# Optimization experiments

Measured on AMD Instinct MI355X. Metric: run time of the kernel, lower is better.

Reference implementation:

```python
import jax, jax.numpy as jnp
import numpy as np

B, T = 128, 512
V, P, K = 10002, 500, 20
DC, DP, DT = 300, 100, 50
D = DC + DP + DT
H = 256


def setup_inputs() -> dict:
    key = jax.random.key(0)
    ks = jax.random.split(key, 21)
    s = lambda i, shape: jax.random.normal(ks[i], shape, jnp.float32) * 0.05
    return dict(
        x=jax.random.randint(ks[0], (B, T), 0, V),
        y=jax.random.randint(ks[1], (B, T), 0, K),
        pre_tags=jax.random.randint(ks[2], (B, T), 0, K),
        pinyin_tags=jax.random.randint(ks[3], (B, T), 0, P),
        mask=jnp.ones((B, T), bool),
        char_emb=s(4, (V, DC)),
        tag_emb=s(5, (K, DT)),
        pinyin_emb=s(6, (P, DP)),
        w_ih_f=s(7, (4 * H, D)), w_hh_f=s(8, (4 * H, H)), b_ih_f=s(9, (4 * H,)), b_hh_f=s(10, (4 * H,)),
        w_ih_b=s(11, (4 * H, D)), w_hh_b=s(12, (4 * H, H)), b_ih_b=s(13, (4 * H,)), b_hh_b=s(14, (4 * H,)),
        w_out=s(15, (K, 2 * H)), b_out=s(16, (K,)),
        start_trans=s(17, (K,)), end_trans=s(18, (K,)), trans=s(19, (K, K)),
    )


def _lstm_dir(xs, w_ih, w_hh, b_ih, b_hh, reverse):
    # xs: [T,B,D]; precompute input projection for all steps (one big GEMM)
    pre = jnp.einsum('tbd,gd->tbg', xs, w_ih) + b_ih + b_hh  # [T,B,4H]
    bsz = xs.shape[1]

    def step(carry, gx):
        h, c = carry
        g = gx + h @ w_hh.T
        i, f, gg, o = jnp.split(g, 4, axis=-1)  # torch gate order i,f,g,o
        c = jax.nn.sigmoid(f) * c + jax.nn.sigmoid(i) * jnp.tanh(gg)
        h = jax.nn.sigmoid(o) * jnp.tanh(c)
        return (h, c), h

    init = (jnp.zeros((bsz, H), xs.dtype), jnp.zeros((bsz, H), xs.dtype))
    _, hs = jax.lax.scan(step, init, pre, reverse=reverse)
    return hs  # [T,B,H]


def _emissions(x, pre_tags, pinyin_tags, char_emb, tag_emb, pinyin_emb,
               w_ih_f, w_hh_f, b_ih_f, b_hh_f, w_ih_b, w_hh_b, b_ih_b, b_hh_b,
               w_out, b_out):
    emb = jnp.concatenate([char_emb[x], pinyin_emb[pinyin_tags], tag_emb[pre_tags]], axis=2)  # [B,T,D]
    xs = emb.transpose(1, 0, 2)  # [T,B,D]
    hf = _lstm_dir(xs, w_ih_f, w_hh_f, b_ih_f, b_hh_f, reverse=False)
    hb = _lstm_dir(xs, w_ih_b, w_hh_b, b_ih_b, b_hh_b, reverse=True)
    h = jnp.concatenate([hf, hb], axis=-1)  # [T,B,2H]
    return jnp.einsum('tbh,kh->tbk', h, w_out) + b_out  # emissions [T,B,K]


def _crf_nll(em, tags, mask, start, trans, end):
    # em [T,B,K] (time-major), torchcrf forward with reduction='sum'
    tg = tags.T  # [T,B]
    mk = mask.T.astype(em.dtype)  # [T,B]
    # gold-path score
    first = start[tg[0]] + jnp.take_along_axis(em[0], tg[0][:, None], 1)[:, 0]

    def num_step(score, inputs):
        e_t, t_prev, t_cur, m = inputs
        s = trans[t_prev, t_cur] + jnp.take_along_axis(e_t, t_cur[:, None], 1)[:, 0]
        return score + s * m, None

    score, _ = jax.lax.scan(num_step, first, (em[1:], tg[:-1], tg[1:], mk[1:]))
    last_idx = (mask.sum(1) - 1).astype(jnp.int32)
    last_tag = jnp.take_along_axis(tags, last_idx[:, None].astype(tags.dtype), 1)[:, 0]
    score = score + end[last_tag]
    # partition function via forward algorithm
    alpha0 = start[None, :] + em[0]  # [B,K]

    def den_step(alpha, inputs):
        e_t, m = inputs
        nxt = jax.nn.logsumexp(alpha[:, :, None] + trans[None, :, :] + e_t[:, None, :], axis=1)
        return jnp.where(m[:, None] > 0, nxt, alpha), None

    alpha, _ = jax.lax.scan(den_step, alpha0, (em[1:], mk[1:]))
    logZ = jax.nn.logsumexp(alpha + end[None, :], axis=1)
    llh = jnp.sum(score - logZ)
    return -llh  # module returns -crf(...)


def reference(x, y, pre_tags, pinyin_tags, mask, char_emb, tag_emb, pinyin_emb,
              w_ih_f, w_hh_f, b_ih_f, b_hh_f, w_ih_b, w_hh_b, b_ih_b, b_hh_b,
              w_out, b_out, start_trans, end_trans, trans):
    em = _emissions(x, pre_tags, pinyin_tags, char_emb, tag_emb, pinyin_emb,
                    w_ih_f, w_hh_f, b_ih_f, b_hh_f, w_ih_b, w_hh_b, b_ih_b, b_hh_b,
                    w_out, b_out)
    return _crf_nll(em, y, mask, start_trans, trans, end_trans)
```

## Files before the change

kernel.cpp:

```cpp
#include <hip/hip_runtime.h>
#include <hip/hip_bf16.h>

typedef __attribute__((ext_vector_type(8))) short short8;
typedef __attribute__((ext_vector_type(4))) float float4v;

#if __has_builtin(__builtin_amdgcn_sdot4)
#define DOT4(a, b, c) __builtin_amdgcn_sdot4((int)(a), (int)(b), (c), false)
#else
__device__ __forceinline__ int dot4_(int a, int b, int c) {
  c += (int)(signed char)(a) * (int)(signed char)(b);
  c += (int)(signed char)(a >> 8) * (int)(signed char)(b >> 8);
  c += (int)(signed char)(a >> 16) * (int)(signed char)(b >> 16);
  c += (a >> 24) * (b >> 24);
  return c;
}
#define DOT4(a, b, c) dot4_((int)(a), (int)(b), (c))
#endif

__device__ __forceinline__ float sigmoidf_(float x) {
  return __fdividef(1.f, 1.f + __expf(-x));
}
__device__ __forceinline__ float tanhf_(float x) {
  float e = __expf(2.f * x);
  return 1.f - __fdividef(2.f, e + 1.f);
}
__device__ __forceinline__ float bflo(unsigned int v) {
  return __uint_as_float(v << 16);
}
__device__ __forceinline__ float bfhi(unsigned int v) {
  return __uint_as_float(v & 0xffff0000u);
}
__device__ __forceinline__ void barrier_lgkm() {
  asm volatile("s_waitcnt lgkmcnt(0)\n\ts_barrier" ::: "memory");
}

template <int CTRL>
__device__ __forceinline__ int qadd_i(int v) {
  return v + __builtin_amdgcn_update_dpp(0, v, CTRL, 0xF, 0xF, true);
}
#define XOR1 0xB1
#define XOR2 0x4E

__device__ __forceinline__ unsigned int pack4_(float4 v, float inv) {
  int b0 = (int)rintf(v.x * inv), b1 = (int)rintf(v.y * inv);
  int b2 = (int)rintf(v.z * inv), b3 = (int)rintf(v.w * inv);
  return (unsigned int)((b0 & 0xff) | ((b1 & 0xff) << 8) | ((b2 & 0xff) << 16) |
                        ((b3 & 0xff) << 24));
}

__global__ __launch_bounds__(256) void wquant_kernel(
    const float* __restrict__ whh_f, const float* __restrict__ whh_b,
    unsigned int* __restrict__ wq, float* __restrict__ wsc) {
  const int wave_g = blockIdx.x * 4 + (threadIdx.x >> 6);
  const int lane = threadIdx.x & 63;
  const int dir = wave_g >> 10, row = wave_g & 1023;
  const float* __restrict__ src = (dir ? whh_b : whh_f) + (size_t)row * 256;
  float4 v = ((const float4*)src)[lane];
  float mx = fmaxf(fmaxf(fabsf(v.x), fabsf(v.y)), fmaxf(fabsf(v.z), fabsf(v.w)));
#pragma unroll
  for (int k = 32; k >= 1; k >>= 1) mx = fmaxf(mx, __shfl_xor(mx, k, 64));
  float inv = (mx > 0.f) ? __fdividef(127.f, mx) : 0.f;
  wq[(size_t)wave_g * 64 + lane] = pack4_(v, inv);
  if (lane == 0) wsc[wave_g] = (mx > 0.f) ? (mx / (127.f * 127.f)) : 0.f;
}

__global__ __launch_bounds__(256) void proj_gemm(
    const float* __restrict__ A, int rowsA, int Kdim, int col_off,
    const float* __restrict__ wf, const float* __restrict__ wb,
    const float* __restrict__ bf1, const float* __restrict__ bf2,
    const float* __restrict__ bb1, const float* __restrict__ bb2,
    __hip_bfloat16* __restrict__ out, int add_bias) {
  __shared__ __align__(16) __hip_bfloat16 As[128][40];
  __shared__ __align__(16) __hip_bfloat16 Bs[256][40];
  const int tid = threadIdx.x;
  const int m0 = blockIdx.x * 128, n0 = blockIdx.y * 256;
  const int lane = tid & 63, wave = tid >> 6;
  const int quad = lane >> 4, lm = lane & 15;
  float4v acc[2][16] = {};
  const int ksteps = (Kdim + 31) >> 5;
  const int r2 = tid >> 1, cbase = (tid & 1) << 4;
  const int rb = tid >> 4, cb = (tid & 15) * 2;
  for (int ks = 0; ks < ksteps; ++ks) {
    const int k0 = ks << 5;
#pragma unroll
    for (int e2 = 0; e2 < 8; ++e2) {
      int kk = k0 + cbase + 2 * e2;
      float b0 = 0.f, b1 = 0.f;
      if (m0 + r2 < rowsA && kk < Kdim) {
        float2 v = *(const float2*)(A + (size_t)(m0 + r2) * Kdim + kk);
        b0 = v.x;
        b1 = v.y;
      }
      As[r2][cbase + 2 * e2] = __float2bfloat16(b0);
      As[r2][cbase + 2 * e2 + 1] = __float2bfloat16(b1);
    }
#pragma unroll
    for (int j = 0; j < 16; ++j) {
      int n = n0 + rb + 16 * j;
      const float* __restrict__ wrow =
          (n < 1024) ? (wf + n * 450 + col_off) : (wb + (n - 1024) * 450 + col_off);
      int kk = k0 + cb;
      float b0 = 0.f, b1 = 0.f;
      if (kk < Kdim) {
        float2 v = *(const float2*)(wrow + kk);
        b0 = v.x;
        b1 = v.y;
      }
      Bs[rb + 16 * j][cb] = __float2bfloat16(b0);
      Bs[rb + 16 * j][cb + 1] = __float2bfloat16(b1);
    }
    __syncthreads();
    short8 af0 = *(const short8*)(&As[wave * 32 + lm][quad * 8]);
    short8 af1 = *(const short8*)(&As[wave * 32 + 16 + lm][quad * 8]);
#pragma unroll
    for (int t = 0; t < 16; ++t) {
      short8 bf = *(const short8*)(&Bs[t * 16 + lm][quad * 8]);
      acc[0][t] = __builtin_amdgcn_mfma_f32_16x16x32_bf16(af0, bf, acc[0][t], 0, 0, 0);
      acc[1][t] = __builtin_amdgcn_mfma_f32_16x16x32_bf16(af1, bf, acc[1][t], 0, 0, 0);
    }
    __syncthreads();
  }
#pragma unroll
  for (int mg = 0; mg < 2; ++mg) {
#pragma unroll
    for (int t = 0; t < 16; ++t) {
#pragma unroll
      for (int rr = 0; rr < 4; ++rr) {
        int m = m0 + wave * 32 + mg * 16 + quad * 4 + rr;
        int col = n0 + t * 16 + lm;
        if (m < rowsA) {
          float v = acc[mg][t][rr];
          if (add_bias)
            v += (col < 1024) ? (bf1[col] + bf2[col]) : (bb1[col - 1024] + bb2[col - 1024]);
          int dir = col >> 10, rq = col & 1023;
          int gate = rq >> 8, u = rq & 255;
          out[m * 2048 + dir * 1024 + u * 4 + gate] = __float2bfloat16(v);
        }
      }
    }
  }
}

__global__ __launch_bounds__(512, 2) void lstm_kernel(
    const unsigned int* __restrict__ wq, const float* __restrict__ wsc,
    const int* __restrict__ x, const int* __restrict__ ptags, const int* __restrict__ gtags,
    const char* __restrict__ char_proj, const char* __restrict__ pin_proj,
    const char* __restrict__ tag_proj, __hip_bfloat16* __restrict__ h_out) {
  extern __shared__ __align__(16) char smem[];
  __hip_bfloat16* hist = (__hip_bfloat16*)smem;
  signed char* hb = (signed char*)(smem + 16384);

  const int tid = threadIdx.x;
  const int q = tid >> 2, e = tid & 3;
  const int chain = blockIdx.x;
  const int dir = chain >> 7;
  const int b = chain & 127;
  const int boff = b * 512;

  if (tid < 32) ((int4*)hb)[tid] = make_int4(0, 0, 0, 0);

  int rslot = tid;
  asm volatile("" : "+v"(rslot));

  const unsigned int* __restrict__ wqd = wq + (size_t)dir * 65536;
  const float* __restrict__ wscd = wsc + dir * 1024;
  const int sub_e = e & 1;
  const int u_mine = 2 * q + sub_e;

  unsigned int Wreg[8][16];
  {
    uint4* lbuf = (uint4*)smem;
#pragma unroll
    for (int rr = 0; rr < 8; ++rr) {
      const int g = rr & 3, sub = rr >> 2;
      const int grow = g * 256 + 2 * q + sub;
      const uint4* __restrict__ srcp = (const uint4*)(wqd + grow * 64 + e * 16);
#pragma unroll
      for (int c = 0; c < 4; ++c) {
        lbuf[tid] = srcp[c];
        uint4 a = lbuf[rslot];
        Wreg[rr][4 * c + 0] = a.x;
        Wreg[rr][4 * c + 1] = a.y;
        Wreg[rr][4 * c + 2] = a.z;
        Wreg[rr][4 * c + 3] = a.w;
      }
    }
  }
  float sc4[4];
  {
    float* fl = (float*)(smem + 8192);
#pragma unroll
    for (int g = 0; g < 4; ++g) {
      fl[tid] = wscd[g * 256 + u_mine];
      sc4[g] = fl[rslot];
    }
  }
  __syncthreads();

  const int pre_off = dir * 2048 + u_mine * 8;
  float cst = 0.f;

  int t_cur = dir ? 511 : 0;
  int t_nxt = dir ? 510 : 1;
  int xc = x[boff + t_cur], pc_i = ptags[boff + t_cur], gc_i = gtags[boff + t_cur];
  uint2 vc = *(const uint2*)(char_proj + (size_t)xc * 4096 + pre_off);
  uint2 vp = *(const uint2*)(pin_proj + (size_t)pc_i * 4096 + pre_off);
  uint2 vg = *(const uint2*)(tag_proj + (size_t)gc_i * 4096 + pre_off);
  int xn = x[boff + t_nxt], pn = ptags[boff + t_nxt], gn = gtags[boff + t_nxt];

  for (int s = 0; s < 512; ++s) {
    const uint2 cv = vc, pv = vp, gv = vg;
    const int t_fut = dir ? (t_nxt > 0 ? t_nxt - 1 : 0) : (t_nxt < 511 ? t_nxt + 1 : 511);
    vc = *(const uint2*)(char_proj + (size_t)xn * 4096 + pre_off);
    vp = *(const uint2*)(pin_proj + (size_t)pn * 4096 + pre_off);
    vg = *(const uint2*)(tag_proj + (size_t)gn * 4096 + pre_off);
    xn = x[boff + t_fut];
    pn = ptags[boff + t_fut];
    gn = gtags[boff + t_fut];

    const signed char* hbase = hb + (s & 1) * 256 + e * 64;
    int acc[8] = {0, 0, 0, 0, 0, 0, 0, 0};
#pragma unroll
    for (int c = 0; c < 4; ++c) {
      uint4 H = *(const uint4*)(hbase + c * 16);
#pragma unroll
      for (int rr = 0; rr < 8; ++rr) {
        acc[rr] = DOT4(Wreg[rr][4 * c + 0], H.x, acc[rr]);
        acc[rr] = DOT4(Wreg[rr][4 * c + 1], H.y, acc[rr]);
        acc[rr] = DOT4(Wreg[rr][4 * c + 2], H.z, acc[rr]);
        acc[rr] = DOT4(Wreg[rr][4 * c + 3], H.w, acc[rr]);
      }
    }
#pragma unroll
    for (int rr = 0; rr < 8; ++rr) {
      int v = qadd_i<XOR1>(acc[rr]);
      acc[rr] = qadd_i<XOR2>(v);
    }
    int ai = sub_e ? acc[4] : acc[0];
    int af = sub_e ? acc[5] : acc[1];
    int ag = sub_e ? acc[6] : acc[2];
    int ao = sub_e ? acc[7] : acc[3];
    float gi = bflo(cv.x) + bflo(pv.x) + bflo(gv.x) + (float)ai * sc4[0];
    float gf = bfhi(cv.x) + bfhi(pv.x) + bfhi(gv.x) + (float)af * sc4[1];
    float gg = bflo(cv.y) + bflo(pv.y) + bflo(gv.y) + (float)ag * sc4[2];
    float go = bfhi(cv.y) + bfhi(pv.y) + bfhi(gv.y) + (float)ao * sc4[3];
    cst = sigmoidf_(gf) * cst + sigmoidf_(gi) * tanhf_(gg);
    float hval = sigmoidf_(go) * tanhf_(cst);
    if (e < 2) {
      hb[((s + 1) & 1) * 256 + u_mine] = (signed char)(int)rintf(hval * 127.f);
      hist[(s & 31) * 256 + u_mine] = __float2bfloat16(hval);
    }
    barrier_lgkm();
    if ((s & 15) == 15) {
      const int slotBase = (s & 31) & ~15;
      const int sBase = s - 15;
      const int row = tid >> 5;
      const int col16 = tid & 31;
      uint4 v = *(const uint4*)((const char*)hist + (slotBase + row) * 512 + col16 * 16);
      int step_r = sBase + row;
      int t_r = dir ? (511 - step_r) : step_r;
      *(uint4*)((char*)h_out + ((size_t)(chain * 512 + t_r) * 256) * 2 + col16 * 16) = v;
    }
    t_cur = t_nxt;
    t_nxt = t_fut;
  }
}

__global__ __launch_bounds__(256) void emis_kernel(
    const __hip_bfloat16* __restrict__ h_glob, const float* __restrict__ w_out,
    const float* __restrict__ b_out, float* __restrict__ em) {
  __shared__ __align__(16) __hip_bfloat16 As[64][40];
  __shared__ __align__(16) __hip_bfloat16 Bs[32][40];
  const int tid = threadIdx.x;
  const int n0 = blockIdx.x * 64;
  const int lane = tid & 63, wave = tid >> 6, quad = lane >> 4, lm = lane & 15;
  float4v acc[2] = {};
  const int r = tid >> 2, c0 = (tid & 3) << 3;
  const int rb = tid >> 3, cb = (tid & 7) << 2;
  for (int ks = 0; ks < 16; ++ks) {
    const int j0 = ks * 32;
    const int dirk = j0 >> 8, jin = j0 & 255;
    const int n = n0 + r, bb = n >> 9, tt = n & 511;
    const uint4* src =
        (const uint4*)(h_glob + ((size_t)(dirk * 128 + bb) * 512 + tt) * 256 + jin + c0);
    *(uint4*)(&As[r][c0]) = *src;
#pragma unroll
    for (int e = 0; e < 4; ++e) {
      float v = (rb < 20) ? w_out[rb * 512 + j0 + cb + e] : 0.f;
      Bs[rb][cb + e] = __float2bfloat16(v);
    }
    __syncthreads();
    short8 af = *(const short8*)(&As[wave * 16 + lm][quad * 8]);
#pragma unroll
    for (int t2 = 0; t2 < 2; ++t2) {
      short8 bf = *(const short8*)(&Bs[t2 * 16 + lm][quad * 8]);
      acc[t2] = __builtin_amdgcn_mfma_f32_16x16x32_bf16(af, bf, acc[t2], 0, 0, 0);
    }
    __syncthreads();
  }
#pragma unroll
  for (int t2 = 0; t2 < 2; ++t2) {
#pragma unroll
    for (int rr = 0; rr < 4; ++rr) {
      int col = t2 * 16 + lm;
      if (col < 20) {
        int n = n0 + wave * 16 + quad * 4 + rr;
        em[(size_t)n * 20 + col] = acc[t2][rr] + b_out[col];
      }
    }
  }
}

__global__ __launch_bounds__(64) void crf_kernel(
    const float* __restrict__ em, const int* __restrict__ y,
    const float* __restrict__ start_trans, const float* __restrict__ end_trans,
    const float* __restrict__ trans, float* __restrict__ partials) {
  const int b = blockIdx.x;
  const int lane = threadIdx.x;
  const int jj = lane < 20 ? lane : 19;
  const bool act = lane < 20;
  const float* __restrict__ emb = em + (size_t)b * 512 * 20;
  const int* __restrict__ yb = y + b * 512;

  float s_part = 0.f;
#pragma unroll
  for (int i = 0; i < 8; ++i) {
    int t = lane + 64 * i;
    int yc = yb[t];
    float v = emb[t * 20 + yc];
    v += (t == 0) ? start_trans[yc] : trans[yb[t - 1] * 20 + yc];
    s_part += v;
  }
#pragma unroll
  for (int k = 32; k >= 1; k >>= 1) s_part += __shfl_xor(s_part, k, 64);
  float score = s_part + end_trans[yb[511]];

  float ET[20];
#pragma unroll
  for (int i = 0; i < 20; ++i) ET[i] = __expf(trans[i * 20 + jj]);
  float alpha = act ? (start_trans[jj] + emb[jj]) : -1e30f;
  float P = alpha;
#pragma unroll
  for (int k = 32; k >= 1; k >>= 1) P = fmaxf(P, __shfl_xor(P, k, 64));

  float eC = emb[1 * 20 + jj];
  float eN = emb[2 * 20 + jj];
  for (int t = 1; t < 512; ++t) {
    if ((t & 15) == 0) {
      P = alpha;
#pragma unroll
      for (int k = 32; k >= 1; k >>= 1) P = fmaxf(P, __shfl_xor(P, k, 64));
    }
    float ex = __expf(alpha - P);
    float s0 = 0.f, s1 = 0.f;
#pragma unroll
    for (int i = 0; i < 20; i += 2) {
      float e0 = __int_as_float(__builtin_amdgcn_readlane(__float_as_int(ex), i));
      float e1 = __int_as_float(__builtin_amdgcn_readlane(__float_as_int(ex), i + 1));
      s0 = fmaf(e0, ET[i], s0);
      s1 = fmaf(e1, ET[i + 1], s1);
    }
    int tf = t + 2 < 512 ? t + 2 : 511;
    float eF = emb[tf * 20 + jj];
    if (act) alpha = P + __logf(s0 + s1) + eC;
    eC = eN;
    eN = eF;
  }
  float v = act ? (alpha + end_trans[jj]) : -1e30f;
  float Pz = v;
#pragma unroll
  for (int k = 32; k >= 1; k >>= 1) Pz = fmaxf(Pz, __shfl_xor(Pz, k, 64));
  float e2 = __expf(v - Pz);
#pragma unroll
  for (int k = 32; k >= 1; k >>= 1) e2 += __shfl_xor(e2, k, 64);
  float logZ = Pz + __logf(e2);
  if (lane == 0) partials[b] = logZ - score;
}

__global__ __launch_bounds__(128) void reduce_kernel(const float* __restrict__ partials,
                                                     float* __restrict__ out) {
  const int tid = threadIdx.x;
  float v = partials[tid];
#pragma unroll
  for (int k = 32; k >= 1; k >>= 1) v += __shfl_xor(v, k, 64);
  __shared__ float tmp[2];
  if ((tid & 63) == 0) tmp[tid >> 6] = v;
  __syncthreads();
  if (tid == 0) out[0] = tmp[0] + tmp[1];
}

extern "C" void kernel_launch(void* const* d_in, const int* in_sizes, int n_in,
                              void* d_out, int out_size, void* d_ws, size_t ws_size,
                              hipStream_t stream) {
  const int* x = (const int*)d_in[0];
  const int* y = (const int*)d_in[1];
  const int* pre_tags = (const int*)d_in[2];
  const int* pinyin_tags = (const int*)d_in[3];
  const float* char_emb = (const float*)d_in[5];
  const float* tag_emb = (const float*)d_in[6];
  const float* pinyin_emb = (const float*)d_in[7];
  const float* w_ih_f = (const float*)d_in[8];
  const float* w_hh_f = (const float*)d_in[9];
  const float* b_ih_f = (const float*)d_in[10];
  const float* b_hh_f = (const float*)d_in[11];
  const float* w_ih_b = (const float*)d_in[12];
  const float* w_hh_b = (const float*)d_in[13];
  const float* b_ih_b = (const float*)d_in[14];
  const float* b_hh_b = (const float*)d_in[15];
  const float* w_out = (const float*)d_in[16];
  const float* b_out = (const float*)d_in[17];
  const float* start_trans = (const float*)d_in[18];
  const float* end_trans = (const float*)d_in[19];
  const float* trans = (const float*)d_in[20];

  char* ws = (char*)d_ws;
  __hip_bfloat16* char_proj = (__hip_bfloat16*)(ws);
  __hip_bfloat16* pin_proj = (__hip_bfloat16*)(ws + 40968192);
  __hip_bfloat16* tag_proj = (__hip_bfloat16*)(ws + 43016192);
  __hip_bfloat16* h_glob = (__hip_bfloat16*)(ws + 43098112);
  float* em = (float*)(ws + 110206976);
  float* partials = (float*)(ws + 115449856);
  unsigned int* wq = (unsigned int*)(ws + 110206976);
  float* wsc = (float*)(ws + 110206976 + 524288);

  wquant_kernel<<<512, 256, 0, stream>>>(w_hh_f, w_hh_b, wq, wsc);

  proj_gemm<<<dim3(79, 8), 256, 0, stream>>>(char_emb, 10002, 300, 0, w_ih_f, w_ih_b,
                                             nullptr, nullptr, nullptr, nullptr, char_proj, 0);
  proj_gemm<<<dim3(4, 8), 256, 0, stream>>>(pinyin_emb, 500, 100, 300, w_ih_f, w_ih_b,
                                            nullptr, nullptr, nullptr, nullptr, pin_proj, 0);
  proj_gemm<<<dim3(1, 8), 256, 0, stream>>>(tag_emb, 20, 50, 400, w_ih_f, w_ih_b,
                                            b_ih_f, b_hh_f, b_ih_b, b_hh_b, tag_proj, 1);

  const int lstm_lds = 16896;
  hipFuncSetAttribute((const void*)lstm_kernel, hipFuncAttributeMaxDynamicSharedMemorySize,
                      lstm_lds);
  lstm_kernel<<<256, 512, lstm_lds, stream>>>(wq, wsc, x, pinyin_tags, pre_tags,
                                              (const char*)char_proj, (const char*)pin_proj,
                                              (const char*)tag_proj, h_glob);

  emis_kernel<<<1024, 256, 0, stream>>>(h_glob, w_out, b_out, em);
  crf_kernel<<<128, 64, 0, stream>>>(em, y, start_trans, end_trans, trans, partials);
  reduce_kernel<<<1, 128, 0, stream>>>(partials, (float*)d_out);
}
```

Baseline: 1.088 ms.

## Batch 16 LSTM chains per block using int8 MFMA for recurrent matvec

Replaces the per-chain LSTM recurrence, which used one block per sequence with sdot4 dot products and DPP reductions, with blocks that each handle 16 batch elements of one direction. The recurrent step becomes an int8 16x16x64 MFMA GEMM with weights held in MFMA fragment registers. The grid shrinks from 256 blocks to 16, so the 512 sequential steps run on far fewer CUs. In exchange each step does dense matrix work with better weight reuse, at the cost of more work per block per step and less parallelism across the device.

```diff
diff --git a/kernel.cpp b/kernel.cpp
--- a/kernel.cpp
+++ b/kernel.cpp
@@ -3,19 +3,7 @@
 
 typedef __attribute__((ext_vector_type(8))) short short8;
 typedef __attribute__((ext_vector_type(4))) float float4v;
-
-#if __has_builtin(__builtin_amdgcn_sdot4)
-#define DOT4(a, b, c) __builtin_amdgcn_sdot4((int)(a), (int)(b), (c), false)
-#else
-__device__ __forceinline__ int dot4_(int a, int b, int c) {
-  c += (int)(signed char)(a) * (int)(signed char)(b);
-  c += (int)(signed char)(a >> 8) * (int)(signed char)(b >> 8);
-  c += (int)(signed char)(a >> 16) * (int)(signed char)(b >> 16);
-  c += (a >> 24) * (b >> 24);
-  return c;
-}
-#define DOT4(a, b, c) dot4_((int)(a), (int)(b), (c))
-#endif
+typedef __attribute__((ext_vector_type(4))) int int4v;
 
 __device__ __forceinline__ float sigmoidf_(float x) {
   return __fdividef(1.f, 1.f + __expf(-x));
@@ -33,19 +21,17 @@
 __device__ __forceinline__ void barrier_lgkm() {
   asm volatile("s_waitcnt lgkmcnt(0)\n\ts_barrier" ::: "memory");
 }
-
-template <int CTRL>
-__device__ __forceinline__ int qadd_i(int v) {
-  return v + __builtin_amdgcn_update_dpp(0, v, CTRL, 0xF, 0xF, true);
-}
-#define XOR1 0xB1
-#define XOR2 0x4E
 
 __device__ __forceinline__ unsigned int pack4_(float4 v, float inv) {
   int b0 = (int)rintf(v.x * inv), b1 = (int)rintf(v.y * inv);
   int b2 = (int)rintf(v.z * inv), b3 = (int)rintf(v.w * inv);
   return (unsigned int)((b0 & 0xff) | ((b1 & 0xff) << 8) | ((b2 & 0xff) << 16) |
                         ((b3 & 0xff) << 24));
+}
+
+__device__ __forceinline__ unsigned short bf16bits_(float v) {
+  __hip_bfloat16 b = __float2bfloat16(v);
+  return *(unsigned short*)&b;
 }
 
 __global__ __launch_bounds__(256) void wquant_kernel(
@@ -147,122 +133,121 @@
     const char* __restrict__ char_proj, const char* __restrict__ pin_proj,
     const char* __restrict__ tag_proj, __hip_bfloat16* __restrict__ h_out) {
   extern __shared__ __align__(16) char smem[];
-  __hip_bfloat16* hist = (__hip_bfloat16*)smem;
-  signed char* hb = (signed char*)(smem + 16384);
+  char* hqb = smem;
+  char* histb = smem + 8704;
+  float* wscL = (float*)(smem + 42496);
 
   const int tid = threadIdx.x;
-  const int q = tid >> 2, e = tid & 3;
-  const int chain = blockIdx.x;
-  const int dir = chain >> 7;
-  const int b = chain & 127;
-  const int boff = b * 512;
-
-  if (tid < 32) ((int4*)hb)[tid] = make_int4(0, 0, 0, 0);
-
-  int rslot = tid;
-  asm volatile("" : "+v"(rslot));
+  const int w = tid >> 6, lane = tid & 63;
+  const int lm = lane & 15, quad = lane >> 4;
+  const int blk = blockIdx.x;
+  const int dir = blk >> 3, bg = blk & 7;
+  const int bb = bg * 16 + lm;
+  const int b512 = bb * 512;
+
+  for (int i = tid; i < 1024; i += 512) wscL[i] = wsc[dir * 1024 + i];
+  for (int i = tid; i < 2176; i += 512) ((unsigned int*)hqb)[i] = 0u;
 
   const unsigned int* __restrict__ wqd = wq + (size_t)dir * 65536;
-  const float* __restrict__ wscd = wsc + dir * 1024;
-  const int sub_e = e & 1;
-  const int u_mine = 2 * q + sub_e;
-
-  unsigned int Wreg[8][16];
-  {
-    uint4* lbuf = (uint4*)smem;
-#pragma unroll
-    for (int rr = 0; rr < 8; ++rr) {
-      const int g = rr & 3, sub = rr >> 2;
-      const int grow = g * 256 + 2 * q + sub;
-      const uint4* __restrict__ srcp = (const uint4*)(wqd + grow * 64 + e * 16);
-#pragma unroll
-      for (int c = 0; c < 4; ++c) {
-        lbuf[tid] = srcp[c];
-        uint4 a = lbuf[rslot];
-        Wreg[rr][4 * c + 0] = a.x;
-        Wreg[rr][4 * c + 1] = a.y;
-        Wreg[rr][4 * c + 2] = a.z;
-        Wreg[rr][4 * c + 3] = a.w;
+  int4v Wf[4][2][4];
+#pragma unroll
+  for (int g = 0; g < 4; ++g)
+#pragma unroll
+    for (int h = 0; h < 2; ++h) {
+      const int row = g * 256 + w * 32 + h * 16 + lm;
+#pragma unroll
+      for (int kt = 0; kt < 4; ++kt)
+        Wf[g][h][kt] = *(const int4v*)(wqd + row * 64 + kt * 16 + quad * 4);
+    }
+  __syncthreads();
+
+  float c8[2][4] = {};
+  const size_t preoff0 = (size_t)dir * 2048 + (size_t)(w * 32 + quad * 4) * 8;
+
+  int t = dir ? 511 : 0;
+  int xi = x[b512 + t], pi = ptags[b512 + t], gi_ = gtags[b512 + t];
+
+  for (int s = 0; s < 512; ++s) {
+    const int cur = s & 1, nxt = cur ^ 1;
+    const char* cb0 = char_proj + (size_t)xi * 4096 + preoff0;
+    const char* pb0 = pin_proj + (size_t)pi * 4096 + preoff0;
+    const char* tb0 = tag_proj + (size_t)gi_ * 4096 + preoff0;
+    uint4 pc0[2], pp0[2], pt0[2];
+    pc0[0] = *(const uint4*)(cb0);      pc0[1] = *(const uint4*)(cb0 + 16);
+    pp0[0] = *(const uint4*)(pb0);      pp0[1] = *(const uint4*)(pb0 + 16);
+    pt0[0] = *(const uint4*)(tb0);      pt0[1] = *(const uint4*)(tb0 + 16);
+    int sn = (s + 1 < 512) ? s + 1 : 511;
+    int tn = dir ? 511 - sn : sn;
+    int xin = x[b512 + tn], pin_ = ptags[b512 + tn], gin = gtags[b512 + tn];
+
+    int4v acc[4][2] = {};
+    const char* hqcur = hqb + cur * 4352 + lm * 272;
+#pragma unroll
+    for (int kt = 0; kt < 4; ++kt) {
+      int4v Bv = *(const int4v*)(hqcur + kt * 64 + quad * 16);
+#pragma unroll
+      for (int g = 0; g < 4; ++g)
+#pragma unroll
+        for (int h = 0; h < 2; ++h)
+          acc[g][h] = __builtin_amdgcn_mfma_i32_16x16x64_i8(Wf[g][h][kt], Bv, acc[g][h], 0, 0, 0);
+    }
+    uint4 pc1[2], pp1[2], pt1[2];
+    pc1[0] = *(const uint4*)(cb0 + 128); pc1[1] = *(const uint4*)(cb0 + 144);
+    pp1[0] = *(const uint4*)(pb0 + 128); pp1[1] = *(const uint4*)(pb0 + 144);
+    pt1[0] = *(const uint4*)(tb0 + 128); pt1[1] = *(const uint4*)(tb0 + 144);
+
+    char* hqn = hqb + nxt * 4352 + lm * 272 + w * 32 + quad * 4;
+    char* histp = histb + (s & 3) * 8448 + lm * 528 + (size_t)(w * 32 + quad * 4) * 2;
+
+#pragma unroll
+    for (int h = 0; h < 2; ++h) {
+      const float4 s0 = *(const float4*)&wscL[0 * 256 + w * 32 + h * 16 + quad * 4];
+      const float4 s1 = *(const float4*)&wscL[1 * 256 + w * 32 + h * 16 + quad * 4];
+      const float4 s2 = *(const float4*)&wscL[2 * 256 + w * 32 + h * 16 + quad * 4];
+      const float4 s3 = *(const float4*)&wscL[3 * 256 + w * 32 + h * 16 + quad * 4];
+      unsigned int hqpack = 0, hist0 = 0, hist1 = 0;
+#pragma unroll
+      for (int rr = 0; rr < 4; ++rr) {
+        uint4 cc = h ? pc1[rr >> 1] : pc0[rr >> 1];
+        uint4 pp = h ? pp1[rr >> 1] : pp0[rr >> 1];
+        uint4 tt = h ? pt1[rr >> 1] : pt0[rr >> 1];
+        unsigned lo_c = (rr & 1) ? cc.z : cc.x, hi_c = (rr & 1) ? cc.w : cc.y;
+        unsigned lo_p = (rr & 1) ? pp.z : pp.x, hi_p = (rr & 1) ? pp.w : pp.y;
+        unsigned lo_t = (rr & 1) ? tt.z : tt.x, hi_t = (rr & 1) ? tt.w : tt.y;
+        float sci = (rr == 0) ? s0.x : (rr == 1) ? s0.y : (rr == 2) ? s0.z : s0.w;
+        float scf = (rr == 0) ? s1.x : (rr == 1) ? s1.y : (rr == 2) ? s1.z : s1.w;
+        float scg = (rr == 0) ? s2.x : (rr == 1) ? s2.y : (rr == 2) ? s2.z : s2.w;
+        float sco = (rr == 0) ? s3.x : (rr == 1) ? s3.y : (rr == 2) ? s3.z : s3.w;
+        float vi = bflo(lo_c) + bflo(lo_p) + bflo(lo_t) + (float)acc[0][h][rr] * sci;
+        float vf = bfhi(lo_c) + bfhi(lo_p) + bfhi(lo_t) + (float)acc[1][h][rr] * scf;
+        float vg = bflo(hi_c) + bflo(hi_p) + bflo(hi_t) + (float)acc[2][h][rr] * scg;
+        float vo = bfhi(hi_c) + bfhi(hi_p) + bfhi(hi_t) + (float)acc[3][h][rr] * sco;
+        float c = sigmoidf_(vf) * c8[h][rr] + sigmoidf_(vi) * tanhf_(vg);
+        c8[h][rr] = c;
+        float hv = sigmoidf_(vo) * tanhf_(c);
+        hqpack |= ((unsigned)((int)rintf(hv * 127.f) & 0xff)) << (8 * rr);
+        unsigned hb = (unsigned)bf16bits_(hv);
+        if (rr < 2) hist0 |= hb << (16 * rr);
+        else hist1 |= hb << (16 * (rr - 2));
       }
-    }
-  }
-  float sc4[4];
-  {
-    float* fl = (float*)(smem + 8192);
-#pragma unroll
-    for (int g = 0; g < 4; ++g) {
-      fl[tid] = wscd[g * 256 + u_mine];
-      sc4[g] = fl[rslot];
-    }
-  }
-  __syncthreads();
-
-  const int pre_off = dir * 2048 + u_mine * 8;
-  float cst = 0.f;
-
-  int t_cur = dir ? 511 : 0;
-  int t_nxt = dir ? 510 : 1;
-  int xc = x[boff + t_cur], pc_i = ptags[boff + t_cur], gc_i = gtags[boff + t_cur];
-  uint2 vc = *(const uint2*)(char_proj + (size_t)xc * 4096 + pre_off);
-  uint2 vp = *(const uint2*)(pin_proj + (size_t)pc_i * 4096 + pre_off);
-  uint2 vg = *(const uint2*)(tag_proj + (size_t)gc_i * 4096 + pre_off);
-  int xn = x[boff + t_nxt], pn = ptags[boff + t_nxt], gn = gtags[boff + t_nxt];
-
-  for (int s = 0; s < 512; ++s) {
-    const uint2 cv = vc, pv = vp, gv = vg;
-    const int t_fut = dir ? (t_nxt > 0 ? t_nxt - 1 : 0) : (t_nxt < 511 ? t_nxt + 1 : 511);
-    vc = *(const uint2*)(char_proj + (size_t)xn * 4096 + pre_off);
-    vp = *(const uint2*)(pin_proj + (size_t)pn * 4096 + pre_off);
-    vg = *(const uint2*)(tag_proj + (size_t)gn * 4096 + pre_off);
-    xn = x[boff + t_fut];
-    pn = ptags[boff + t_fut];
-    gn = gtags[boff + t_fut];
-
-    const signed char* hbase = hb + (s & 1) * 256 + e * 64;
-    int acc[8] = {0, 0, 0, 0, 0, 0, 0, 0};
-#pragma unroll
-    for (int c = 0; c < 4; ++c) {
-      uint4 H = *(const uint4*)(hbase + c * 16);
-#pragma unroll
-      for (int rr = 0; rr < 8; ++rr) {
-        acc[rr] = DOT4(Wreg[rr][4 * c + 0], H.x, acc[rr]);
-        acc[rr] = DOT4(Wreg[rr][4 * c + 1], H.y, acc[rr]);
-        acc[rr] = DOT4(Wreg[rr][4 * c + 2], H.z, acc[rr]);
-        acc[rr] = DOT4(Wreg[rr][4 * c + 3], H.w, acc[rr]);
-      }
-    }
-#pragma unroll
-    for (int rr = 0; rr < 8; ++rr) {
-      int v = qadd_i<XOR1>(acc[rr]);
-      acc[rr] = qadd_i<XOR2>(v);
-    }
-    int ai = sub_e ? acc[4] : acc[0];
-    int af = sub_e ? acc[5] : acc[1];
-    int ag = sub_e ? acc[6] : acc[2];
-    int ao = sub_e ? acc[7] : acc[3];
-    float gi = bflo(cv.x) + bflo(pv.x) + bflo(gv.x) + (float)ai * sc4[0];
-    float gf = bfhi(cv.x) + bfhi(pv.x) + bfhi(gv.x) + (float)af * sc4[1];
-    float gg = bflo(cv.y) + bflo(pv.y) + bflo(gv.y) + (float)ag * sc4[2];
-    float go = bfhi(cv.y) + bfhi(pv.y) + bfhi(gv.y) + (float)ao * sc4[3];
-    cst = sigmoidf_(gf) * cst + sigmoidf_(gi) * tanhf_(gg);
-    float hval = sigmoidf_(go) * tanhf_(cst);
-    if (e < 2) {
-      hb[((s + 1) & 1) * 256 + u_mine] = (signed char)(int)rintf(hval * 127.f);
-      hist[(s & 31) * 256 + u_mine] = __float2bfloat16(hval);
+      *(unsigned int*)(hqn + h * 16) = hqpack;
+      *(uint2*)(histp + h * 32) = make_uint2(hist0, hist1);
     }
     barrier_lgkm();
-    if ((s & 15) == 15) {
-      const int slotBase = (s & 31) & ~15;
-      const int sBase = s - 15;
-      const int row = tid >> 5;
-      const int col16 = tid & 31;
-      uint4 v = *(const uint4*)((const char*)hist + (slotBase + row) * 512 + col16 * 16);
-      int step_r = sBase + row;
-      int t_r = dir ? (511 - step_r) : step_r;
-      *(uint4*)((char*)h_out + ((size_t)(chain * 512 + t_r) * 256) * 2 + col16 * 16) = v;
-    }
-    t_cur = t_nxt;
-    t_nxt = t_fut;
+    if ((s & 3) == 3) {
+      const int row = tid >> 3;
+      const int sr = row >> 4, bi = row & 15;
+      const int step_r = s - 3 + sr;
+      const int t_r = dir ? 511 - step_r : step_r;
+      const char* src = histb + (size_t)(sr * 16 + bi) * 528 + (tid & 7) * 64;
+      char* dst = (char*)h_out +
+                  ((size_t)((dir * 128 + bg * 16 + bi) * 512 + t_r) * 256) * 2 + (tid & 7) * 64;
+#pragma unroll
+      for (int j = 0; j < 4; ++j)
+        ((uint4*)dst)[j] = ((const uint4*)src)[j];
+      barrier_lgkm();
+    }
+    xi = xin; pi = pin_; gi_ = gin; t = tn;
   }
 }
 
@@ -432,12 +417,12 @@
   proj_gemm<<<dim3(1, 8), 256, 0, stream>>>(tag_emb, 20, 50, 400, w_ih_f, w_ih_b,
                                             b_ih_f, b_hh_f, b_ih_b, b_hh_b, tag_proj, 1);
 
-  const int lstm_lds = 16896;
+  const int lstm_lds = 46592;
   hipFuncSetAttribute((const void*)lstm_kernel, hipFuncAttributeMaxDynamicSharedMemorySize,
                       lstm_lds);
-  lstm_kernel<<<256, 512, lstm_lds, stream>>>(wq, wsc, x, pinyin_tags, pre_tags,
-                                              (const char*)char_proj, (const char*)pin_proj,
-                                              (const char*)tag_proj, h_glob);
+  lstm_kernel<<<16, 512, lstm_lds, stream>>>(wq, wsc, x, pinyin_tags, pre_tags,
+                                             (const char*)char_proj, (const char*)pin_proj,
+                                             (const char*)tag_proj, h_glob);
 
   emis_kernel<<<1024, 256, 0, stream>>>(h_glob, w_out, b_out, em);
   crf_kernel<<<128, 64, 0, stream>>>(em, y, start_trans, end_trans, trans, partials);
```

Result: slower. 3.051 ms (+180.3%).

## Double LSTM block threads so each quad computes one hidden unit

Applied to the files above, without the earlier changes.

The recurrent LSTM kernel now launches 1024 threads per chain instead of 512. Each 4-thread group owns a single hidden unit with its 4 gate rows (64 registers of int8 weights) instead of two units. This halves the per-thread dot-product work and weight register footprint per step. In exchange, the block-wide barrier now spans twice as many waves, and the output writeback is limited to the first 512 threads.

```diff
diff --git a/kernel.cpp b/kernel.cpp
--- a/kernel.cpp
+++ b/kernel.cpp
@@ -141,7 +141,7 @@
   }
 }
 
-__global__ __launch_bounds__(512, 2) void lstm_kernel(
+__global__ __launch_bounds__(1024, 4) void lstm_kernel(
     const unsigned int* __restrict__ wq, const float* __restrict__ wsc,
     const int* __restrict__ x, const int* __restrict__ ptags, const int* __restrict__ gtags,
     const char* __restrict__ char_proj, const char* __restrict__ pin_proj,
@@ -164,40 +164,38 @@
 
   const unsigned int* __restrict__ wqd = wq + (size_t)dir * 65536;
   const float* __restrict__ wscd = wsc + dir * 1024;
-  const int sub_e = e & 1;
-  const int u_mine = 2 * q + sub_e;
-
-  unsigned int Wreg[8][16];
+
+  float sc4[4];
+  {
+    float* fl = (float*)smem;
+#pragma unroll
+    for (int g = 0; g < 4; ++g) {
+      fl[tid] = wscd[g * 256 + q];
+      sc4[g] = fl[rslot];
+    }
+  }
+  __syncthreads();
+
+  unsigned int Wreg[4][16];
   {
     uint4* lbuf = (uint4*)smem;
 #pragma unroll
-    for (int rr = 0; rr < 8; ++rr) {
-      const int g = rr & 3, sub = rr >> 2;
-      const int grow = g * 256 + 2 * q + sub;
-      const uint4* __restrict__ srcp = (const uint4*)(wqd + grow * 64 + e * 16);
+    for (int g = 0; g < 4; ++g) {
+      const uint4* __restrict__ srcp = (const uint4*)(wqd + (g * 256 + q) * 64 + e * 16);
 #pragma unroll
       for (int c = 0; c < 4; ++c) {
         lbuf[tid] = srcp[c];
         uint4 a = lbuf[rslot];
-        Wreg[rr][4 * c + 0] = a.x;
-        Wreg[rr][4 * c + 1] = a.y;
-        Wreg[rr][4 * c + 2] = a.z;
-        Wreg[rr][4 * c + 3] = a.w;
-      }
-    }
-  }
-  float sc4[4];
-  {
-    float* fl = (float*)(smem + 8192);
-#pragma unroll
-    for (int g = 0; g < 4; ++g) {
-      fl[tid] = wscd[g * 256 + u_mine];
-      sc4[g] = fl[rslot];
+        Wreg[g][4 * c + 0] = a.x;
+        Wreg[g][4 * c + 1] = a.y;
+        Wreg[g][4 * c + 2] = a.z;
+        Wreg[g][4 * c + 3] = a.w;
+      }
     }
   }
   __syncthreads();
 
-  const int pre_off = dir * 2048 + u_mine * 8;
+  const int pre_off = dir * 2048 + q * 8;
   float cst = 0.f;
 
   int t_cur = dir ? 511 : 0;
@@ -219,47 +217,45 @@
     gn = gtags[boff + t_fut];
 
     const signed char* hbase = hb + (s & 1) * 256 + e * 64;
-    int acc[8] = {0, 0, 0, 0, 0, 0, 0, 0};
+    int acc[4] = {0, 0, 0, 0};
 #pragma unroll
     for (int c = 0; c < 4; ++c) {
       uint4 H = *(const uint4*)(hbase + c * 16);
 #pragma unroll
-      for (int rr = 0; rr < 8; ++rr) {
-        acc[rr] = DOT4(Wreg[rr][4 * c + 0], H.x, acc[rr]);
-        acc[rr] = DOT4(Wreg[rr][4 * c + 1], H.y, acc[rr]);
-        acc[rr] = DOT4(Wreg[rr][4 * c + 2], H.z, acc[rr]);
-        acc[rr] = DOT4(Wreg[rr][4 * c + 3], H.w, acc[rr]);
-      }
-    }
-#pragma unroll
-    for (int rr = 0; rr < 8; ++rr) {
-      int v = qadd_i<XOR1>(acc[rr]);
-      acc[rr] = qadd_i<XOR2>(v);
-    }
-    int ai = sub_e ? acc[4] : acc[0];
-    int af = sub_e ? acc[5] : acc[1];
-    int ag = sub_e ? acc[6] : acc[2];
-    int ao = sub_e ? acc[7] : acc[3];
-    float gi = bflo(cv.x) + bflo(pv.x) + bflo(gv.x) + (float)ai * sc4[0];
-    float gf = bfhi(cv.x) + bfhi(pv.x) + bfhi(gv.x) + (float)af * sc4[1];
-    float gg = bflo(cv.y) + bflo(pv.y) + bflo(gv.y) + (float)ag * sc4[2];
-    float go = bfhi(cv.y) + bfhi(pv.y) + bfhi(gv.y) + (float)ao * sc4[3];
+      for (int g = 0; g < 4; ++g) {
+        acc[g] = DOT4(Wreg[g][4 * c + 0], H.x, acc[g]);
+        acc[g] = DOT4(Wreg[g][4 * c + 1], H.y, acc[g]);
+        acc[g] = DOT4(Wreg[g][4 * c + 2], H.z, acc[g]);
+        acc[g] = DOT4(Wreg[g][4 * c + 3], H.w, acc[g]);
+      }
+    }
+#pragma unroll
+    for (int g = 0; g < 4; ++g) {
+      int v = qadd_i<XOR1>(acc[g]);
+      acc[g] = qadd_i<XOR2>(v);
+    }
+    float gi = bflo(cv.x) + bflo(pv.x) + bflo(gv.x) + (float)acc[0] * sc4[0];
+    float gf = bfhi(cv.x) + bfhi(pv.x) + bfhi(gv.x) + (float)acc[1] * sc4[1];
+    float gg = bflo(cv.y) + bflo(pv.y) + bflo(gv.y) + (float)acc[2] * sc4[2];
+    float go = bfhi(cv.y) + bfhi(pv.y) + bfhi(gv.y) + (float)acc[3] * sc4[3];
     cst = sigmoidf_(gf) * cst + sigmoidf_(gi) * tanhf_(gg);
     float hval = sigmoidf_(go) * tanhf_(cst);
-    if (e < 2) {
-      hb[((s + 1) & 1) * 256 + u_mine] = (signed char)(int)rintf(hval * 127.f);
-      hist[(s & 31) * 256 + u_mine] = __float2bfloat16(hval);
+    if (e == 0) {
+      hb[((s + 1) & 1) * 256 + q] = (signed char)(int)rintf(hval * 127.f);
+      hist[(s & 31) * 256 + q] = __float2bfloat16(hval);
     }
     barrier_lgkm();
     if ((s & 15) == 15) {
-      const int slotBase = (s & 31) & ~15;
-      const int sBase = s - 15;
-      const int row = tid >> 5;
-      const int col16 = tid & 31;
-      uint4 v = *(const uint4*)((const char*)hist + (slotBase + row) * 512 + col16 * 16);
-      int step_r = sBase + row;
-      int t_r = dir ? (511 - step_r) : step_r;
-      *(uint4*)((char*)h_out + ((size_t)(chain * 512 + t_r) * 256) * 2 + col16 * 16) = v;
+      if (tid < 512) {
+        const int slotBase = (s & 31) & ~15;
+        const int sBase = s - 15;
+        const int row = tid >> 5;
+        const int col16 = tid & 31;
+        uint4 v = *(const uint4*)((const char*)hist + (slotBase + row) * 512 + col16 * 16);
+        int step_r = sBase + row;
+        int t_r = dir ? (511 - step_r) : step_r;
+        *(uint4*)((char*)h_out + ((size_t)(chain * 512 + t_r) * 256) * 2 + col16 * 16) = v;
+      }
     }
     t_cur = t_nxt;
     t_nxt = t_fut;
@@ -435,9 +431,9 @@
   const int lstm_lds = 16896;
   hipFuncSetAttribute((const void*)lstm_kernel, hipFuncAttributeMaxDynamicSharedMemorySize,
                       lstm_lds);
-  lstm_kernel<<<256, 512, lstm_lds, stream>>>(wq, wsc, x, pinyin_tags, pre_tags,
-                                              (const char*)char_proj, (const char*)pin_proj,
-                                              (const char*)tag_proj, h_glob);
+  lstm_kernel<<<256, 1024, lstm_lds, stream>>>(wq, wsc, x, pinyin_tags, pre_tags,
+                                               (const char*)char_proj, (const char*)pin_proj,
+                                               (const char*)tag_proj, h_glob);
 
   emis_kernel<<<1024, 256, 0, stream>>>(h_glob, w_out, b_out, em);
   crf_kernel<<<128, 64, 0, stream>>>(em, y, start_trans, end_trans, trans, partials);
```

Result: slower. 1.286 ms (+18.1%).

## Use int8 MFMA for LSTM recurrent matvec instead of sdot4 with DPP reductions

Applied to the files above, without the earlier changes.

Replaces the per-lane sdot4 dot products and quad DPP reductions in the recurrent step with int8 MFMA 16x16x64 instructions. Weights are held in registers as MFMA A-fragments and the quantized hidden state is the B operand. Only one of the 16 output columns is meaningful, so most of each MFMA's work is wasted, and the per-step latency may rise because of MFMA dependency chains. The hidden-state buffer is padded to 272 bytes per slot and the unit-to-lane mapping is rearranged to match the MFMA output layout.

```diff
diff --git a/kernel.cpp b/kernel.cpp
--- a/kernel.cpp
+++ b/kernel.cpp
@@ -3,19 +3,7 @@
 
 typedef __attribute__((ext_vector_type(8))) short short8;
 typedef __attribute__((ext_vector_type(4))) float float4v;
-
-#if __has_builtin(__builtin_amdgcn_sdot4)
-#define DOT4(a, b, c) __builtin_amdgcn_sdot4((int)(a), (int)(b), (c), false)
-#else
-__device__ __forceinline__ int dot4_(int a, int b, int c) {
-  c += (int)(signed char)(a) * (int)(signed char)(b);
-  c += (int)(signed char)(a >> 8) * (int)(signed char)(b >> 8);
-  c += (int)(signed char)(a >> 16) * (int)(signed char)(b >> 16);
-  c += (a >> 24) * (b >> 24);
-  return c;
-}
-#define DOT4(a, b, c) dot4_((int)(a), (int)(b), (c))
-#endif
+typedef __attribute__((ext_vector_type(4))) int int4v;
 
 __device__ __forceinline__ float sigmoidf_(float x) {
   return __fdividef(1.f, 1.f + __expf(-x));
@@ -33,19 +21,18 @@
 __device__ __forceinline__ void barrier_lgkm() {
   asm volatile("s_waitcnt lgkmcnt(0)\n\ts_barrier" ::: "memory");
 }
-
-template <int CTRL>
-__device__ __forceinline__ int qadd_i(int v) {
-  return v + __builtin_amdgcn_update_dpp(0, v, CTRL, 0xF, 0xF, true);
-}
-#define XOR1 0xB1
-#define XOR2 0x4E
 
 __device__ __forceinline__ unsigned int pack4_(float4 v, float inv) {
   int b0 = (int)rintf(v.x * inv), b1 = (int)rintf(v.y * inv);
   int b2 = (int)rintf(v.z * inv), b3 = (int)rintf(v.w * inv);
   return (unsigned int)((b0 & 0xff) | ((b1 & 0xff) << 8) | ((b2 & 0xff) << 16) |
                         ((b3 & 0xff) << 24));
+}
+
+__device__ __forceinline__ int sel4_(int4v v, int rr) {
+  int a = (rr & 1) ? v[1] : v[0];
+  int b = (rr & 1) ? v[3] : v[2];
+  return (rr & 2) ? b : a;
 }
 
 __global__ __launch_bounds__(256) void wquant_kernel(
@@ -148,56 +135,38 @@
     const char* __restrict__ tag_proj, __hip_bfloat16* __restrict__ h_out) {
   extern __shared__ __align__(16) char smem[];
   __hip_bfloat16* hist = (__hip_bfloat16*)smem;
-  signed char* hb = (signed char*)(smem + 16384);
+  char* hqb = smem + 16384;
 
   const int tid = threadIdx.x;
-  const int q = tid >> 2, e = tid & 3;
+  const int w = tid >> 6, lane = tid & 63;
+  const int quad = lane >> 4, lm = lane & 15;
+  const int sel = lm >> 1;
+  const int mt = sel >> 2, rr = sel & 3;
+  const int unit = w * 32 + mt * 16 + quad * 4 + rr;
   const int chain = blockIdx.x;
   const int dir = chain >> 7;
   const int b = chain & 127;
   const int boff = b * 512;
 
-  if (tid < 32) ((int4*)hb)[tid] = make_int4(0, 0, 0, 0);
-
-  int rslot = tid;
-  asm volatile("" : "+v"(rslot));
+  if (tid < 34) ((uint4*)hqb)[tid] = make_uint4(0, 0, 0, 0);
 
   const unsigned int* __restrict__ wqd = wq + (size_t)dir * 65536;
-  const float* __restrict__ wscd = wsc + dir * 1024;
-  const int sub_e = e & 1;
-  const int u_mine = 2 * q + sub_e;
-
-  unsigned int Wreg[8][16];
-  {
-    uint4* lbuf = (uint4*)smem;
-#pragma unroll
-    for (int rr = 0; rr < 8; ++rr) {
-      const int g = rr & 3, sub = rr >> 2;
-      const int grow = g * 256 + 2 * q + sub;
-      const uint4* __restrict__ srcp = (const uint4*)(wqd + grow * 64 + e * 16);
-#pragma unroll
-      for (int c = 0; c < 4; ++c) {
-        lbuf[tid] = srcp[c];
-        uint4 a = lbuf[rslot];
-        Wreg[rr][4 * c + 0] = a.x;
-        Wreg[rr][4 * c + 1] = a.y;
-        Wreg[rr][4 * c + 2] = a.z;
-        Wreg[rr][4 * c + 3] = a.w;
-      }
-    }
-  }
+  int4v Wf[4][2][4];
+#pragma unroll
+  for (int g = 0; g < 4; ++g)
+#pragma unroll
+    for (int m = 0; m < 2; ++m) {
+      const int row = g * 256 + w * 32 + m * 16 + lm;
+#pragma unroll
+      for (int kt = 0; kt < 4; ++kt)
+        Wf[g][m][kt] = *(const int4v*)(wqd + row * 64 + kt * 16 + quad * 4);
+    }
   float sc4[4];
-  {
-    float* fl = (float*)(smem + 8192);
-#pragma unroll
-    for (int g = 0; g < 4; ++g) {
-      fl[tid] = wscd[g * 256 + u_mine];
-      sc4[g] = fl[rslot];
-    }
-  }
+#pragma unroll
+  for (int g = 0; g < 4; ++g) sc4[g] = wsc[dir * 1024 + g * 256 + unit];
   __syncthreads();
 
-  const int pre_off = dir * 2048 + u_mine * 8;
+  const int pre_off = dir * 2048 + unit * 8;
   float cst = 0.f;
 
   int t_cur = dir ? 511 : 0;
@@ -209,6 +178,7 @@
   int xn = x[boff + t_nxt], pn = ptags[boff + t_nxt], gn = gtags[boff + t_nxt];
 
   for (int s = 0; s < 512; ++s) {
+    const int cur = s & 1, nxt = cur ^ 1;
     const uint2 cv = vc, pv = vp, gv = vg;
     const int t_fut = dir ? (t_nxt > 0 ? t_nxt - 1 : 0) : (t_nxt < 511 ? t_nxt + 1 : 511);
     vc = *(const uint2*)(char_proj + (size_t)xn * 4096 + pre_off);
@@ -218,37 +188,31 @@
     pn = ptags[boff + t_fut];
     gn = gtags[boff + t_fut];
 
-    const signed char* hbase = hb + (s & 1) * 256 + e * 64;
-    int acc[8] = {0, 0, 0, 0, 0, 0, 0, 0};
-#pragma unroll
-    for (int c = 0; c < 4; ++c) {
-      uint4 H = *(const uint4*)(hbase + c * 16);
-#pragma unroll
-      for (int rr = 0; rr < 8; ++rr) {
-        acc[rr] = DOT4(Wreg[rr][4 * c + 0], H.x, acc[rr]);
-        acc[rr] = DOT4(Wreg[rr][4 * c + 1], H.y, acc[rr]);
-        acc[rr] = DOT4(Wreg[rr][4 * c + 2], H.z, acc[rr]);
-        acc[rr] = DOT4(Wreg[rr][4 * c + 3], H.w, acc[rr]);
-      }
-    }
-#pragma unroll
-    for (int rr = 0; rr < 8; ++rr) {
-      int v = qadd_i<XOR1>(acc[rr]);
-      acc[rr] = qadd_i<XOR2>(v);
-    }
-    int ai = sub_e ? acc[4] : acc[0];
-    int af = sub_e ? acc[5] : acc[1];
-    int ag = sub_e ? acc[6] : acc[2];
-    int ao = sub_e ? acc[7] : acc[3];
+    int4v acc[4][2] = {};
+    const char* hqc = hqb + cur * 272;
+#pragma unroll
+    for (int kt = 0; kt < 4; ++kt) {
+      int4v Bv = *(const int4v*)(hqc + kt * 64 + quad * 16);
+#pragma unroll
+      for (int g = 0; g < 4; ++g)
+#pragma unroll
+        for (int m = 0; m < 2; ++m)
+          acc[g][m] = __builtin_amdgcn_mfma_i32_16x16x64_i8(Wf[g][m][kt], Bv, acc[g][m], 0, 0, 0);
+    }
+
+    int ai = mt ? sel4_(acc[0][1], rr) : sel4_(acc[0][0], rr);
+    int af = mt ? sel4_(acc[1][1], rr) : sel4_(acc[1][0], rr);
+    int ag = mt ? sel4_(acc[2][1], rr) : sel4_(acc[2][0], rr);
+    int ao = mt ? sel4_(acc[3][1], rr) : sel4_(acc[3][0], rr);
     float gi = bflo(cv.x) + bflo(pv.x) + bflo(gv.x) + (float)ai * sc4[0];
     float gf = bfhi(cv.x) + bfhi(pv.x) + bfhi(gv.x) + (float)af * sc4[1];
     float gg = bflo(cv.y) + bflo(pv.y) + bflo(gv.y) + (float)ag * sc4[2];
     float go = bfhi(cv.y) + bfhi(pv.y) + bfhi(gv.y) + (float)ao * sc4[3];
     cst = sigmoidf_(gf) * cst + sigmoidf_(gi) * tanhf_(gg);
     float hval = sigmoidf_(go) * tanhf_(cst);
-    if (e < 2) {
-      hb[((s + 1) & 1) * 256 + u_mine] = (signed char)(int)rintf(hval * 127.f);
-      hist[(s & 31) * 256 + u_mine] = __float2bfloat16(hval);
+    if (!(lm & 1)) {
+      ((signed char*)hqb)[nxt * 272 + unit] = (signed char)(int)rintf(hval * 127.f);
+      hist[(s & 31) * 256 + unit] = __float2bfloat16(hval);
     }
     barrier_lgkm();
     if ((s & 15) == 15) {
@@ -432,7 +396,7 @@
   proj_gemm<<<dim3(1, 8), 256, 0, stream>>>(tag_emb, 20, 50, 400, w_ih_f, w_ih_b,
                                             b_ih_f, b_hh_f, b_ih_b, b_hh_b, tag_proj, 1);
 
-  const int lstm_lds = 16896;
+  const int lstm_lds = 16928;
   hipFuncSetAttribute((const void*)lstm_kernel, hipFuncAttributeMaxDynamicSharedMemorySize,
                       lstm_lds);
   lstm_kernel<<<256, 512, lstm_lds, stream>>>(wq, wsc, x, pinyin_tags, pre_tags,
```

After: 966.5 us. -11.2%, faster.
